# Performance work log

Measured on AMD Instinct MI355X. Metric: run time of the kernel, lower is better.

The kernel has to match this reference:

```python
import jax, jax.numpy as jnp
import numpy as np

R = 32          # voxel resolution
EPS = 0.0       # normalization eps


def setup_inputs() -> dict:
    key = jax.random.key(0)
    k1, k2 = jax.random.split(key)
    B, D, N = 16, 64, 32768
    features = jax.random.normal(k1, (B, D, N), dtype=jnp.float32)
    coords = jax.random.normal(k2, (B, 3, N), dtype=jnp.float32)
    return {"features": features, "coords": coords}


def reference(features, coords):
    """features: (B, D, N), coords: (B, 3, N).
    Returns (voxel_features (B, D, R, R, R), norm_coords (B, 3, N))."""
    B, D, N = features.shape
    r = R

    # --- normalize coords into [0, r-1] (torch detaches coords; fwd math identical) ---
    nc = coords - coords.mean(axis=2, keepdims=True)                    # center
    norm = jnp.linalg.norm(nc, axis=1, keepdims=True)                   # (B,1,N)
    max_norm = norm.max(axis=2, keepdims=True)                          # (B,1,1)
    nc = nc / (max_norm * 2.0 + EPS) + 0.5
    norm_coords = jnp.clip(nc * r, 0, r - 1)                            # (B,3,N)
    vox = jnp.round(norm_coords).astype(jnp.int32)                      # (B,3,N)

    # --- scatter-mean features into r^3 voxels (avg_voxelize) ---
    idx = vox[:, 0] * (r * r) + vox[:, 1] * r + vox[:, 2]               # (B,N) in [0, r^3)
    flat_idx = (idx + jnp.arange(B, dtype=jnp.int32)[:, None] * (r ** 3)).reshape(-1)  # (B*N,)
    flat_feat = features.transpose(0, 2, 1).reshape(B * N, D)           # (B*N, D)

    sums = jax.ops.segment_sum(flat_feat, flat_idx, num_segments=B * r ** 3)   # (B*r^3, D)
    cnt = jax.ops.segment_sum(jnp.ones((B * N,), dtype=features.dtype),
                              flat_idx, num_segments=B * r ** 3)               # (B*r^3,)
    avg = sums / jnp.maximum(cnt, 1.0)[:, None]                          # empty voxels -> 0

    vox_feat = avg.reshape(B, r ** 3, D).transpose(0, 2, 1).reshape(B, D, r, r, r)
    return vox_feat, norm_coords
```

## Files before the change

### kernel.cpp

```cpp
#include <hip/hip_runtime.h>

#define RES 32
#define R3 (RES * RES * RES)

__device__ __forceinline__ void fadd_native(float* p, float v) {
    unsafeAtomicAdd(p, v);
}

__global__ void sums_kernel(const float* __restrict__ coords,
                            float* __restrict__ accum, int N) {
    const int b = blockIdx.y;
    const int stride = gridDim.x * blockDim.x;
    const float* cb = coords + (size_t)b * 3 * N;
    const int nvec = N >> 2;
    const float4* c0 = (const float4*)cb;
    const float4* c1 = (const float4*)(cb + N);
    const float4* c2 = (const float4*)(cb + 2 * N);

    float s0 = 0.f, s1 = 0.f, s2 = 0.f;
    for (int n = blockIdx.x * blockDim.x + threadIdx.x; n < nvec; n += stride) {
        float4 a = c0[n]; s0 += (a.x + a.y) + (a.z + a.w);
        float4 c = c1[n]; s1 += (c.x + c.y) + (c.z + c.w);
        float4 d = c2[n]; s2 += (d.x + d.y) + (d.z + d.w);
    }
    if (blockIdx.x == 0 && threadIdx.x == 0) {
        for (int n = nvec << 2; n < N; ++n) {
            s0 += cb[n]; s1 += cb[N + n]; s2 += cb[2 * N + n];
        }
    }
    for (int off = 32; off; off >>= 1) {
        s0 += __shfl_down(s0, off);
        s1 += __shfl_down(s1, off);
        s2 += __shfl_down(s2, off);
    }
    __shared__ float r0[4], r1[4], r2[4];
    const int lane = threadIdx.x & 63, wv = threadIdx.x >> 6;
    if (lane == 0) { r0[wv] = s0; r1[wv] = s1; r2[wv] = s2; }
    __syncthreads();
    if (threadIdx.x == 0) {
        float t0 = 0.f, t1 = 0.f, t2 = 0.f;
        const int nw = blockDim.x >> 6;
        for (int w = 0; w < nw; ++w) { t0 += r0[w]; t1 += r1[w]; t2 += r2[w]; }
        fadd_native(&accum[b * 4 + 0], t0);
        fadd_native(&accum[b * 4 + 1], t1);
        fadd_native(&accum[b * 4 + 2], t2);
    }
}

__global__ void maxn_kernel(const float* __restrict__ coords,
                            const float* __restrict__ accum,
                            unsigned* __restrict__ maxsq, int N) {
    const int b = blockIdx.y;
    const int stride = gridDim.x * blockDim.x;
    const float* cb = coords + (size_t)b * 3 * N;
    const float m0 = accum[b * 4 + 0] / (float)N;
    const float m1 = accum[b * 4 + 1] / (float)N;
    const float m2 = accum[b * 4 + 2] / (float)N;
    const int nvec = N >> 2;
    const float4* c0 = (const float4*)cb;
    const float4* c1 = (const float4*)(cb + N);
    const float4* c2 = (const float4*)(cb + 2 * N);

    float mx = 0.f;
    for (int n = blockIdx.x * blockDim.x + threadIdx.x; n < nvec; n += stride) {
        float4 a = c0[n], c = c1[n], d = c2[n];
        a.x -= m0; a.y -= m0; a.z -= m0; a.w -= m0;
        c.x -= m1; c.y -= m1; c.z -= m1; c.w -= m1;
        d.x -= m2; d.y -= m2; d.z -= m2; d.w -= m2;
        mx = fmaxf(mx, a.x * a.x + c.x * c.x + d.x * d.x);
        mx = fmaxf(mx, a.y * a.y + c.y * c.y + d.y * d.y);
        mx = fmaxf(mx, a.z * a.z + c.z * c.z + d.z * d.z);
        mx = fmaxf(mx, a.w * a.w + c.w * c.w + d.w * d.w);
    }
    if (blockIdx.x == 0 && threadIdx.x == 0) {
        for (int n = nvec << 2; n < N; ++n) {
            float a = cb[n] - m0, c = cb[N + n] - m1, d = cb[2 * N + n] - m2;
            mx = fmaxf(mx, a * a + c * c + d * d);
        }
    }
    for (int off = 32; off; off >>= 1) mx = fmaxf(mx, __shfl_down(mx, off));
    __shared__ float r0[4];
    const int lane = threadIdx.x & 63, wv = threadIdx.x >> 6;
    if (lane == 0) r0[wv] = mx;
    __syncthreads();
    if (threadIdx.x == 0) {
        const int nw = blockDim.x >> 6;
        for (int w = 0; w < nw; ++w) mx = fmaxf(mx, r0[w]);
        atomicMax(&maxsq[b], __float_as_uint(mx));
    }
}

__global__ void point_kernel(const float* __restrict__ coords,
                             const float* __restrict__ accum,
                             const unsigned* __restrict__ maxsq,
                             float* __restrict__ nc_out,
                             int* __restrict__ idx_out,
                             int* __restrict__ counts, int N) {
    const int n4 = blockIdx.x * blockDim.x + threadIdx.x;
    const int b = blockIdx.y;
    const int nvec = (N + 3) >> 2;
    if (n4 >= nvec) return;

    const float* cb = coords + (size_t)b * 3 * N;
    const float m0 = accum[b * 4 + 0] / (float)N;
    const float m1 = accum[b * 4 + 1] / (float)N;
    const float m2 = accum[b * 4 + 2] / (float)N;
    const float denom = 2.0f * sqrtf(__uint_as_float(maxsq[b]));
    float* ncb = nc_out + (size_t)b * 3 * N;
    int* irow = idx_out + (size_t)b * N;
    int* crow = counts + (size_t)b * R3;

    const int n0 = n4 << 2;
    if (n0 + 3 < N) {
        float4 a = *(const float4*)(cb + n0);
        float4 c = *(const float4*)(cb + N + n0);
        float4 d = *(const float4*)(cb + 2 * N + n0);
        float4 v0, v1, v2;
        int4 id;
        #define PROC(comp)                                                        \
        {                                                                         \
            float x = (a.comp - m0) / denom + 0.5f;                               \
            float y = (c.comp - m1) / denom + 0.5f;                               \
            float z = (d.comp - m2) / denom + 0.5f;                               \
            v0.comp = fminf(fmaxf(x * (float)RES, 0.f), (float)(RES - 1));        \
            v1.comp = fminf(fmaxf(y * (float)RES, 0.f), (float)(RES - 1));        \
            v2.comp = fminf(fmaxf(z * (float)RES, 0.f), (float)(RES - 1));        \
            id.comp = (int)rintf(v0.comp) * RES * RES                             \
                    + (int)rintf(v1.comp) * RES + (int)rintf(v2.comp);            \
        }
        PROC(x) PROC(y) PROC(z) PROC(w)
        #undef PROC
        *(float4*)(ncb + n0) = v0;
        *(float4*)(ncb + N + n0) = v1;
        *(float4*)(ncb + 2 * N + n0) = v2;
        *(int4*)(irow + n0) = id;
        atomicAdd(&crow[id.x], 1);
        atomicAdd(&crow[id.y], 1);
        atomicAdd(&crow[id.z], 1);
        atomicAdd(&crow[id.w], 1);
    } else {
        for (int n = n0; n < N; ++n) {
            float x = (cb[n] - m0) / denom + 0.5f;
            float y = (cb[N + n] - m1) / denom + 0.5f;
            float z = (cb[2 * N + n] - m2) / denom + 0.5f;
            float v0 = fminf(fmaxf(x * (float)RES, 0.f), (float)(RES - 1));
            float v1 = fminf(fmaxf(y * (float)RES, 0.f), (float)(RES - 1));
            float v2 = fminf(fmaxf(z * (float)RES, 0.f), (float)(RES - 1));
            ncb[n] = v0; ncb[N + n] = v1; ncb[2 * N + n] = v2;
            int id = (int)rintf(v0) * RES * RES + (int)rintf(v1) * RES + (int)rintf(v2);
            irow[n] = id;
            atomicAdd(&crow[id], 1);
        }
    }
}

__global__ __launch_bounds__(1024) void reduce_kernel(
        const float* __restrict__ feats,
        const int* __restrict__ idx,
        const int* __restrict__ counts,
        float* __restrict__ vox, int D, int N) {
    const int d = blockIdx.x;
    const int b = blockIdx.y;
    const int tid = threadIdx.x;

    __shared__ float acc[R3];
    {
        float4* a4 = (float4*)acc;
        const float4 z = make_float4(0.f, 0.f, 0.f, 0.f);
        for (int v = tid; v < (R3 >> 2); v += blockDim.x) a4[v] = z;
    }
    __syncthreads();

    const float* frow = feats + ((size_t)b * D + d) * N;
    const int* irow = idx + (size_t)b * N;
    const int nvec = N >> 2;
    const float4* f4 = (const float4*)frow;
    const int4* i4 = (const int4*)irow;
    for (int n = tid; n < nvec; n += blockDim.x) {
        float4 f = f4[n];
        int4 i = i4[n];
        fadd_native(&acc[i.x], f.x);
        fadd_native(&acc[i.y], f.y);
        fadd_native(&acc[i.z], f.z);
        fadd_native(&acc[i.w], f.w);
    }
    if (tid == 0) {
        for (int n = nvec << 2; n < N; ++n) fadd_native(&acc[irow[n]], frow[n]);
    }
    __syncthreads();

    const int* crow = counts + (size_t)b * R3;
    float* vrow = vox + ((size_t)b * D + d) * R3;
    const int4* c4 = (const int4*)crow;
    float4* v4 = (float4*)vrow;
    for (int v = tid; v < (R3 >> 2); v += blockDim.x) {
        int4 c = c4[v];
        float4 a = ((const float4*)acc)[v];
        a.x /= (float)(c.x > 1 ? c.x : 1);
        a.y /= (float)(c.y > 1 ? c.y : 1);
        a.z /= (float)(c.z > 1 ? c.z : 1);
        a.w /= (float)(c.w > 1 ? c.w : 1);
        v4[v] = a;
    }
}

extern "C" void kernel_launch(void* const* d_in, const int* in_sizes, int n_in,
                              void* d_out, int out_size, void* d_ws, size_t ws_size,
                              hipStream_t stream) {
    const float* feats  = (const float*)d_in[0];
    const float* coords = (const float*)d_in[1];
    float* out = (float*)d_out;

    const int D = (int)(3LL * in_sizes[0] / in_sizes[1]);
    const int B = (int)((long long)(out_size - in_sizes[1]) / ((long long)D * R3));
    const int N = in_sizes[1] / (3 * B);

    float* vox_out = out;
    float* nc_out  = out + (size_t)B * D * R3;

    float*    accum  = (float*)d_ws;
    unsigned* maxsq  = (unsigned*)((char*)d_ws + 1024);
    int*      counts = (int*)((char*)d_ws + 4096);
    int*      idx    = (int*)((char*)d_ws + 4096 + (size_t)B * R3 * sizeof(int));

    hipMemsetAsync(d_ws, 0, 4096 + (size_t)B * R3 * sizeof(int), stream);

    sums_kernel <<<dim3(8, B), dim3(256), 0, stream>>>(coords, accum, N);
    maxn_kernel <<<dim3(8, B), dim3(256), 0, stream>>>(coords, accum, maxsq, N);

    const int nvec = (N + 3) >> 2;
    point_kernel<<<dim3((nvec + 255) / 256, B), dim3(256), 0, stream>>>(
        coords, accum, maxsq, nc_out, idx, counts, N);

    reduce_kernel<<<dim3(D, B), dim3(1024), 0, stream>>>(
        feats, idx, counts, vox_out, D, N);
}
```

Baseline: 395.9 us.

## Replace LDS atomic scatter with counting-sort point lists and per-voxel gather

Adds a prefix-scan kernel and a point-list kernel that bucket point indices by voxel, stored as 16-bit values. The reduce kernel then has each thread gather the features of its voxel's points for two feature channels and divide by the count, instead of scattering with shared-memory float atomics over a 128KB buffer. The aim is to remove LDS atomic contention and the large per-block LDS footprint. In exchange it uses uncoalesced random feature reads, uneven per-thread work because points cluster in central voxels, and two extra launches. It also assumes N fits in 16 bits and D is even, and the coordinate-reduction grids are widened from 8 to 16 blocks.

```diff
diff --git a/kernel.cpp b/kernel.cpp
--- a/kernel.cpp
+++ b/kernel.cpp
@@ -2,10 +2,6 @@
 
 #define RES 32
 #define R3 (RES * RES * RES)
-
-__device__ __forceinline__ void fadd_native(float* p, float v) {
-    unsafeAtomicAdd(p, v);
-}
 
 __global__ void sums_kernel(const float* __restrict__ coords,
                             float* __restrict__ accum, int N) {
@@ -41,9 +37,9 @@
         float t0 = 0.f, t1 = 0.f, t2 = 0.f;
         const int nw = blockDim.x >> 6;
         for (int w = 0; w < nw; ++w) { t0 += r0[w]; t1 += r1[w]; t2 += r2[w]; }
-        fadd_native(&accum[b * 4 + 0], t0);
-        fadd_native(&accum[b * 4 + 1], t1);
-        fadd_native(&accum[b * 4 + 2], t2);
+        unsafeAtomicAdd(&accum[b * 4 + 0], t0);
+        unsafeAtomicAdd(&accum[b * 4 + 1], t1);
+        unsafeAtomicAdd(&accum[b * 4 + 2], t2);
     }
 }
 
@@ -94,7 +90,7 @@
                              const float* __restrict__ accum,
                              const unsigned* __restrict__ maxsq,
                              float* __restrict__ nc_out,
-                             int* __restrict__ idx_out,
+                             unsigned short* __restrict__ idx_out,
                              int* __restrict__ counts, int N) {
     const int n4 = blockIdx.x * blockDim.x + threadIdx.x;
     const int b = blockIdx.y;
@@ -107,7 +103,7 @@
     const float m2 = accum[b * 4 + 2] / (float)N;
     const float denom = 2.0f * sqrtf(__uint_as_float(maxsq[b]));
     float* ncb = nc_out + (size_t)b * 3 * N;
-    int* irow = idx_out + (size_t)b * N;
+    unsigned short* irow = idx_out + (size_t)b * N;
     int* crow = counts + (size_t)b * R3;
 
     const int n0 = n4 << 2;
@@ -133,7 +129,10 @@
         *(float4*)(ncb + n0) = v0;
         *(float4*)(ncb + N + n0) = v1;
         *(float4*)(ncb + 2 * N + n0) = v2;
-        *(int4*)(irow + n0) = id;
+        ushort4 us;
+        us.x = (unsigned short)id.x; us.y = (unsigned short)id.y;
+        us.z = (unsigned short)id.z; us.w = (unsigned short)id.w;
+        *(ushort4*)(irow + n0) = us;
         atomicAdd(&crow[id.x], 1);
         atomicAdd(&crow[id.y], 1);
         atomicAdd(&crow[id.z], 1);
@@ -148,59 +147,102 @@
             float v2 = fminf(fmaxf(z * (float)RES, 0.f), (float)(RES - 1));
             ncb[n] = v0; ncb[N + n] = v1; ncb[2 * N + n] = v2;
             int id = (int)rintf(v0) * RES * RES + (int)rintf(v1) * RES + (int)rintf(v2);
-            irow[n] = id;
+            irow[n] = (unsigned short)id;
             atomicAdd(&crow[id], 1);
         }
     }
+}
+
+__global__ __launch_bounds__(1024) void scan_kernel(
+        const int* __restrict__ counts,
+        int* __restrict__ cursor,
+        unsigned short* __restrict__ start) {
+    const int b = blockIdx.x;
+    const int tid = threadIdx.x;
+    const int lane = tid & 63, wv = tid >> 6;
+    const int base = tid * 32;
+    const int* crow = counts + (size_t)b * R3;
+
+    int vals[32];
+    int tot = 0;
+    const int4* c4 = (const int4*)(crow + base);
+    for (int i = 0; i < 8; ++i) {
+        int4 t = c4[i];
+        vals[4 * i + 0] = t.x; vals[4 * i + 1] = t.y;
+        vals[4 * i + 2] = t.z; vals[4 * i + 3] = t.w;
+        tot += (t.x + t.y) + (t.z + t.w);
+    }
+    int inc = tot;
+    for (int o = 1; o < 64; o <<= 1) {
+        int t = __shfl_up(inc, o);
+        if (lane >= o) inc += t;
+    }
+    __shared__ int wsum[16], woff[16];
+    if (lane == 63) wsum[wv] = inc;
+    __syncthreads();
+    if (tid == 0) {
+        int r = 0;
+        for (int w = 0; w < 16; ++w) { woff[w] = r; r += wsum[w]; }
+    }
+    __syncthreads();
+    int run = woff[wv] + inc - tot;
+    unsigned short* srow = start + (size_t)b * R3 + base;
+    int* urow = cursor + (size_t)b * R3 + base;
+    for (int i = 0; i < 32; ++i) {
+        srow[i] = (unsigned short)run;
+        urow[i] = run;
+        run += vals[i];
+    }
+}
+
+__global__ void plist_kernel(const unsigned short* __restrict__ idx,
+                             int* __restrict__ cursor,
+                             unsigned short* __restrict__ plist, int N) {
+    const int n = blockIdx.x * blockDim.x + threadIdx.x;
+    const int b = blockIdx.y;
+    if (n >= N) return;
+    const int v = idx[(size_t)b * N + n];
+    const int pos = atomicAdd(&cursor[(size_t)b * R3 + v], 1);
+    plist[(size_t)b * N + pos] = (unsigned short)n;
 }
 
 __global__ __launch_bounds__(1024) void reduce_kernel(
         const float* __restrict__ feats,
-        const int* __restrict__ idx,
+        const unsigned short* __restrict__ plist,
+        const unsigned short* __restrict__ start,
         const int* __restrict__ counts,
         float* __restrict__ vox, int D, int N) {
-    const int d = blockIdx.x;
-    const int b = blockIdx.y;
-    const int tid = threadIdx.x;
-
-    __shared__ float acc[R3];
-    {
-        float4* a4 = (float4*)acc;
-        const float4 z = make_float4(0.f, 0.f, 0.f, 0.f);
-        for (int v = tid; v < (R3 >> 2); v += blockDim.x) a4[v] = z;
-    }
-    __syncthreads();
-
-    const float* frow = feats + ((size_t)b * D + d) * N;
-    const int* irow = idx + (size_t)b * N;
-    const int nvec = N >> 2;
-    const float4* f4 = (const float4*)frow;
-    const int4* i4 = (const int4*)irow;
-    for (int n = tid; n < nvec; n += blockDim.x) {
-        float4 f = f4[n];
-        int4 i = i4[n];
-        fadd_native(&acc[i.x], f.x);
-        fadd_native(&acc[i.y], f.y);
-        fadd_native(&acc[i.z], f.z);
-        fadd_native(&acc[i.w], f.w);
-    }
-    if (tid == 0) {
-        for (int n = nvec << 2; n < N; ++n) fadd_native(&acc[irow[n]], frow[n]);
-    }
-    __syncthreads();
-
+    const int d0 = blockIdx.x * 2;
+    const int b = blockIdx.y;
+    const float* frow0 = feats + ((size_t)b * D + d0) * N;
+    const float* frow1 = frow0 + N;
+    const unsigned short* prow = plist + (size_t)b * N;
+    const unsigned short* srow = start + (size_t)b * R3;
     const int* crow = counts + (size_t)b * R3;
-    float* vrow = vox + ((size_t)b * D + d) * R3;
-    const int4* c4 = (const int4*)crow;
-    float4* v4 = (float4*)vrow;
-    for (int v = tid; v < (R3 >> 2); v += blockDim.x) {
-        int4 c = c4[v];
-        float4 a = ((const float4*)acc)[v];
-        a.x /= (float)(c.x > 1 ? c.x : 1);
-        a.y /= (float)(c.y > 1 ? c.y : 1);
-        a.z /= (float)(c.z > 1 ? c.z : 1);
-        a.w /= (float)(c.w > 1 ? c.w : 1);
-        v4[v] = a;
+    float* vrow0 = vox + ((size_t)b * D + d0) * R3;
+    float* vrow1 = vrow0 + R3;
+
+    for (int v = threadIdx.x; v < R3; v += 1024) {
+        const int c = crow[v];
+        const int s = srow[v];
+        float a0 = 0.f, a1 = 0.f;
+        int j = 0;
+        for (; j + 4 <= c; j += 4) {
+            const int p0 = prow[s + j + 0];
+            const int p1 = prow[s + j + 1];
+            const int p2 = prow[s + j + 2];
+            const int p3 = prow[s + j + 3];
+            a0 += (frow0[p0] + frow0[p1]) + (frow0[p2] + frow0[p3]);
+            a1 += (frow1[p0] + frow1[p1]) + (frow1[p2] + frow1[p3]);
+        }
+        for (; j < c; ++j) {
+            const int p = prow[s + j];
+            a0 += frow0[p];
+            a1 += frow1[p];
+        }
+        const float dn = (float)(c > 1 ? c : 1);
+        vrow0[v] = a0 / dn;
+        vrow1[v] = a1 / dn;
     }
 }
 
@@ -218,20 +260,30 @@
     float* vox_out = out;
     float* nc_out  = out + (size_t)B * D * R3;
 
-    float*    accum  = (float*)d_ws;
-    unsigned* maxsq  = (unsigned*)((char*)d_ws + 1024);
-    int*      counts = (int*)((char*)d_ws + 4096);
-    int*      idx    = (int*)((char*)d_ws + 4096 + (size_t)B * R3 * sizeof(int));
-
-    hipMemsetAsync(d_ws, 0, 4096 + (size_t)B * R3 * sizeof(int), stream);
-
-    sums_kernel <<<dim3(8, B), dim3(256), 0, stream>>>(coords, accum, N);
-    maxn_kernel <<<dim3(8, B), dim3(256), 0, stream>>>(coords, accum, maxsq, N);
+    const size_t BR3 = (size_t)B * R3;
+    const size_t BN  = (size_t)B * N;
+    float*          accum  = (float*)d_ws;
+    unsigned*       maxsq  = (unsigned*)((char*)d_ws + 1024);
+    int*            counts = (int*)((char*)d_ws + 4096);
+    int*            cursor = (int*)((char*)d_ws + 4096 + 4 * BR3);
+    unsigned short* start  = (unsigned short*)((char*)d_ws + 4096 + 8 * BR3);
+    unsigned short* idx    = (unsigned short*)((char*)d_ws + 4096 + 10 * BR3);
+    unsigned short* plist  = (unsigned short*)((char*)d_ws + 4096 + 10 * BR3 + 2 * BN);
+
+    hipMemsetAsync(d_ws, 0, 4096 + 4 * BR3, stream);
+
+    sums_kernel <<<dim3(16, B), dim3(256), 0, stream>>>(coords, accum, N);
+    maxn_kernel <<<dim3(16, B), dim3(256), 0, stream>>>(coords, accum, maxsq, N);
 
     const int nvec = (N + 3) >> 2;
     point_kernel<<<dim3((nvec + 255) / 256, B), dim3(256), 0, stream>>>(
         coords, accum, maxsq, nc_out, idx, counts, N);
 
-    reduce_kernel<<<dim3(D, B), dim3(1024), 0, stream>>>(
-        feats, idx, counts, vox_out, D, N);
-}
+    scan_kernel <<<dim3(B), dim3(1024), 0, stream>>>(counts, cursor, start);
+
+    plist_kernel<<<dim3((N + 255) / 256, B), dim3(256), 0, stream>>>(
+        idx, cursor, plist, N);
+
+    reduce_kernel<<<dim3(D / 2, B), dim3(1024), 0, stream>>>(
+        feats, plist, start, counts, vox_out, D, N);
+}
```

New measurement: 708.5 us. 79.0% more time.
